# Optimization experiments

Measured on AMD Instinct MI355X. Metric: run time of the kernel, lower is better.

The kernel has to match this reference:

```python
import jax, jax.numpy as jnp
import numpy as np
from jax import lax

DIM = 192
HEADS = 8
B, H, W = 8, 128, 128


def dwconv3x3(x, w):
    # x: [B,C,H,W], w: [C,1,3,3] depthwise (groups=C)
    return lax.conv_general_dilated(
        x, w, window_strides=(1, 1), padding='SAME',
        feature_group_count=x.shape[1],
        dimension_numbers=('NCHW', 'OIHW', 'NCHW'))


def conv1x1(x, w, b=None):
    # w: [Cout, Cin]
    y = jnp.einsum('oc,bchw->bohw', w, x)
    if b is not None:
        y = y + b[None, :, None, None]
    return y


def setup_inputs() -> dict:
    key = jax.random.key(0)
    ks = jax.random.split(key, 9)
    s = 0.02
    return {
        'x': jax.random.normal(ks[0], (B, DIM, H, W), jnp.float32),
        'w_qkv': jax.random.normal(ks[1], (3 * DIM, DIM), jnp.float32) * s,
        'b_qkv': jnp.zeros((3 * DIM,), jnp.float32),
        'w_dw': jax.random.normal(ks[2], (3 * DIM, 1, 3, 3), jnp.float32) * s,
        'b_dw': jnp.zeros((3 * DIM,), jnp.float32),
        'w_proj': jax.random.normal(ks[3], (DIM, DIM), jnp.float32) * s,
        'b_proj': jnp.zeros((DIM,), jnp.float32),
        'w_pos1': jax.random.normal(ks[4], (DIM, 1, 3, 3), jnp.float32) * s,
        'w_pos2': jax.random.normal(ks[5], (DIM, 1, 3, 3), jnp.float32) * s,
        'temperature': jnp.ones((HEADS, 1, 1), jnp.float32),
    }


def reference(x, w_qkv, b_qkv, w_dw, b_dw, w_proj, b_proj, w_pos1, w_pos2, temperature):
    b, c, h, w = x.shape
    heads = HEADS
    ch = c // heads

    qkv = conv1x1(x, w_qkv, b_qkv)
    qkv = dwconv3x3(qkv, w_dw) + b_dw[None, :, None, None]
    q_inp, k_inp, v_inp = jnp.split(qkv, 3, axis=1)

    def to_heads(t):  # [B,C,H,W] -> [B,heads,ch,HW]
        return t.reshape(b, heads, ch, h * w)

    q = to_heads(q_inp)
    k = to_heads(k_inp)
    v = to_heads(v_inp)

    # L2 normalize over hw (torch F.normalize, eps=1e-12)
    q = q / jnp.maximum(jnp.linalg.norm(q, axis=-1, keepdims=True), 1e-12)
    k = k / jnp.maximum(jnp.linalg.norm(k, axis=-1, keepdims=True), 1e-12)

    attn = jnp.einsum('bhce,bhde->bhcd', q, k) * temperature  # [B,heads,ch,ch]
    attn = jax.nn.softmax(attn, axis=-1)
    out = jnp.einsum('bhcd,bhde->bhce', attn, v)  # [B,heads,ch,HW]
    out = out.reshape(b, c, h, w)

    out = conv1x1(out, w_proj, b_proj)

    pos = dwconv3x3(v_inp, w_pos1)
    pos = jax.nn.gelu(pos, approximate=False)
    pos = dwconv3x3(pos, w_pos2)

    return out + pos
```

## Files before the change

### kernel.cpp

```cpp
#include <hip/hip_runtime.h>
#include <stdint.h>
#include <stddef.h>

#define NB 8
#define CC 192
#define C3 576
#define HGT 128
#define WID 128
#define HW 16384
#define NH 8
#define QKROW 49152

typedef short bf16x8 __attribute__((ext_vector_type(8)));
typedef float f32x4 __attribute__((ext_vector_type(4)));

__device__ __forceinline__ unsigned short f2bf(float f) {
  unsigned int u = __float_as_uint(f);
  u += 0x7fffu + ((u >> 16) & 1u);
  return (unsigned short)(u >> 16);
}
__device__ __forceinline__ float bf2f(unsigned short h) {
  return __uint_as_float(((unsigned int)h) << 16);
}
__device__ __forceinline__ float bflo(unsigned int v) {
  return __uint_as_float(v << 16);
}
__device__ __forceinline__ float bfhi(unsigned int v) {
  return __uint_as_float(v & 0xffff0000u);
}
__device__ __forceinline__ unsigned int pk2(float a, float b) {
  return (unsigned int)f2bf(a) | ((unsigned int)f2bf(b) << 16);
}
__device__ __forceinline__ void gl_lds16(const void* g, void* l) {
  __builtin_amdgcn_global_load_lds(
      (const __attribute__((address_space(1))) unsigned int*)(uintptr_t)g,
      (__attribute__((address_space(3))) unsigned int*)(uint32_t)(uintptr_t)l,
      16, 0, 0);
}
__device__ __forceinline__ int xcd_swz(int g, int n) {
  return (g & 7) * (n >> 3) + (g >> 3);
}

__global__ void kwprep(const float* __restrict__ wq, unsigned char* __restrict__ wb) {
  int f = blockIdx.x * 256 + threadIdx.x;
  if (f >= C3 * 24) return;
  int oc = f / 24, s = f % 24;
  unsigned int wv[4];
#pragma unroll
  for (int j = 0; j < 4; ++j)
    wv[j] = pk2(wq[oc * 192 + s * 8 + 2 * j], wq[oc * 192 + s * 8 + 2 * j + 1]);
  uint4 st; st.x = wv[0]; st.y = wv[1]; st.z = wv[2]; st.w = wv[3];
  *(uint4*)(wb + (size_t)oc * 384 + ((s ^ (oc & 7)) * 16)) = st;
}

__global__ __launch_bounds__(256) void kqkv(const float* __restrict__ x,
                                            const unsigned char* __restrict__ wb,
                                            const float* __restrict__ bqkv,
                                            unsigned short* __restrict__ vout,
                                            unsigned char* __restrict__ qkout) {
  __shared__ __align__(16) unsigned char lds[81920];
  const int ABF = 49152;
  const int TRO = 73728;
  int wg = xcd_swz(blockIdx.x, gridDim.x);
  int t = wg & 255, b = wg >> 8;
  int p0 = t * 64;
  int tid = threadIdx.x;

  const unsigned char* gx = (const unsigned char*)(x + (size_t)b * CC * HW + p0);
#pragma unroll
  for (int i = 0; i < 12; ++i) {
    int f = i * 256 + tid;
    int ch = f >> 4, seg = f & 15;
    gl_lds16(gx + ((size_t)ch * HW + seg * 4) * 4, lds + f * 16);
  }
  asm volatile("s_waitcnt vmcnt(0)" ::: "memory");
  __syncthreads();
  {
    const float* lx = (const float*)lds;
    int p = tid & 63, sg = tid >> 6;
#pragma unroll
    for (int s6 = 0; s6 < 6; ++s6) {
      int s = sg * 6 + s6;
      unsigned int wv[4];
#pragma unroll
      for (int j = 0; j < 4; ++j)
        wv[j] = pk2(lx[(s * 8 + 2 * j) * 64 + p], lx[(s * 8 + 2 * j + 1) * 64 + p]);
      uint4 st; st.x = wv[0]; st.y = wv[1]; st.z = wv[2]; st.w = wv[3];
      *(uint4*)(lds + ABF + (s * 64 + p) * 16) = st;
    }
  }
  __syncthreads();

#pragma unroll
  for (int i = 0; i < 6; ++i)
    gl_lds16(wb + i * 4096 + tid * 16, lds + i * 4096 + tid * 16);

  int lane = tid & 63, w = tid >> 6;
  int l15 = lane & 15, gq = lane >> 4;
  int pw = w * 16;
  int y = t >> 1, xh = (t & 1) * 8;
  int unitw = w * 2 + (gq >> 1);
  int sub8 = (gq & 1) * 8;
  int s4 = w * 4 + gq;
  int ru = tid >> 5, rc0 = tid & 31;
  int vc = tid >> 2, vxq = tid & 3;

  for (int ot = 0; ot < 9; ++ot) {
    if (ot == 0) { asm volatile("s_waitcnt vmcnt(0)" ::: "memory"); }
    else         { asm volatile("s_waitcnt vmcnt(2)" ::: "memory"); }
    __builtin_amdgcn_s_barrier();
    __builtin_amdgcn_sched_barrier(0);
    int nb = ot & 1;
    float bias[4];
#pragma unroll
    for (int nf = 0; nf < 4; ++nf) bias[nf] = bqkv[ot * 64 + nf * 16 + l15];
    if (ot < 8) {
      const unsigned char* gB = wb + (size_t)(ot + 1) * 24576;
#pragma unroll
      for (int i = 0; i < 6; ++i)
        gl_lds16(gB + i * 4096 + tid * 16, lds + (nb ^ 1) * 24576 + i * 4096 + tid * 16);
    }
    f32x4 acc[4];
#pragma unroll
    for (int nf = 0; nf < 4; ++nf) acc[nf] = (f32x4){0.f, 0.f, 0.f, 0.f};
#pragma unroll
    for (int kk = 0; kk < 6; ++kk) {
      bf16x8 a = *(const bf16x8*)(lds + ABF + (((kk * 4 + gq) * 64) + pw + l15) * 16);
      int cb = kk * 64 + gq * 16;
#pragma unroll
      for (int nf = 0; nf < 4; ++nf) {
        int r = nf * 16 + l15;
        bf16x8 bfr = *(const bf16x8*)(lds + nb * 24576 + r * 384 + (cb ^ ((r & 7) << 4)));
        acc[nf] = __builtin_amdgcn_mfma_f32_16x16x32_bf16(a, bfr, acc[nf], 0, 0, 0);
      }
    }
    bool isq = (ot < 6);
    if (isq) {
#pragma unroll
      for (int nf = 0; nf < 4; ++nf) {
        int c = nf * 16 + l15;
        uint2 st;
        st.x = pk2(acc[nf][0] + bias[nf], acc[nf][1] + bias[nf]);
        st.y = pk2(acc[nf][2] + bias[nf], acc[nf][3] + bias[nf]);
        *(uint2*)(lds + TRO + c * 128 + ((unitw ^ (c & 7)) * 16) + sub8) = st;
      }
    } else {
#pragma unroll
      for (int nf = 0; nf < 4; ++nf) {
        int c = nf * 16 + l15;
        uint2 st;
        st.x = pk2(acc[nf][0] + bias[nf], acc[nf][1] + bias[nf]);
        st.y = pk2(acc[nf][2] + bias[nf], acc[nf][3] + bias[nf]);
        *(uint2*)(lds + TRO + c * 128 + ((s4 ^ (c & 15)) * 8)) = st;
      }
    }
    asm volatile("s_waitcnt lgkmcnt(0)" ::: "memory");
    __builtin_amdgcn_s_barrier();
    __builtin_amdgcn_sched_barrier(0);
    if (isq) {
      int part = ot / 3, cm0 = (ot % 3) * 64;
      int c1 = rc0 + 32;
      uint4 v0 = *(const uint4*)(lds + TRO + rc0 * 128 + ((ru ^ (rc0 & 7)) * 16));
      uint4 v1 = *(const uint4*)(lds + TRO + c1 * 128 + ((ru ^ (c1 & 7)) * 16));
      unsigned char* grow = qkout + ((size_t)((part * 8 + b) * 128 + y)) * QKROW +
                            (xh + ru) * 3072 + cm0 * 16;
      *(uint4*)(grow + rc0 * 16) = v0;
      *(uint4*)(grow + c1 * 16) = v1;
    } else {
      uint2 q0 = *(const uint2*)(lds + TRO + vc * 128 + (((4 * vxq + 0) ^ (vc & 15)) * 8));
      uint2 q1 = *(const uint2*)(lds + TRO + vc * 128 + (((4 * vxq + 1) ^ (vc & 15)) * 8));
      uint2 q2 = *(const uint2*)(lds + TRO + vc * 128 + (((4 * vxq + 2) ^ (vc & 15)) * 8));
      uint2 q3 = *(const uint2*)(lds + TRO + vc * 128 + (((4 * vxq + 3) ^ (vc & 15)) * 8));
      unsigned short* vp = vout + ((size_t)(b * CC + (ot - 6) * 64 + vc)) * HW + p0 + vxq * 16;
      uint4 s0; s0.x = q0.x; s0.y = q0.y; s0.z = q1.x; s0.w = q1.y;
      uint4 s1; s1.x = q2.x; s1.y = q2.y; s1.z = q3.x; s1.w = q3.y;
      *(uint4*)vp = s0;
      *(uint4*)(vp + 8) = s1;
    }
  }
}

__global__ __launch_bounds__(256) void kqk(const unsigned char* __restrict__ qk,
                                           const float* __restrict__ wdw,
                                           const float* __restrict__ bdw,
                                           float* __restrict__ G,
                                           float* __restrict__ nq,
                                           float* __restrict__ nk) {
  __shared__ __align__(16) unsigned char lds[49168];
  const int FB = 0;
  const int ZP = 24576;
  const int STG = 24592;
  int wg = xcd_swz(blockIdx.x, gridDim.x);
  int band = wg & 63, h = (wg >> 6) & 7, b = wg >> 9;
  int y0 = band * 2;
  int tid = threadIdx.x;
  if (tid == 0) *(uint4*)(lds + ZP) = (uint4){0, 0, 0, 0};

  int lane = tid & 63, w = tid >> 6;
  int ch = tid >> 3, row = (tid >> 2) & 1, qt = tid & 3;
  int u0 = qt * 4;

#pragma unroll
  for (int p = 0; p < 2; ++p) {
#pragma unroll
    for (int i = 0; i < 6; ++i) {
      int f = i * 256 + tid;
      int r = f / 384, unit = f % 384;
      int uc = unit / 24, cs = unit % 24;
      int yy = y0 - 1 + r;
      if (yy >= 0 && yy < HGT)
        gl_lds16(qk + ((size_t)((p * 8 + b) * 128 + yy)) * QKROW + uc * 3072 + (h * 24 + cs) * 16,
                 lds + STG + f * 16);
      else
        *(uint4*)(lds + STG + f * 16) = (uint4){0, 0, 0, 0};
    }
    asm volatile("s_waitcnt vmcnt(0)" ::: "memory");
    __syncthreads();
    if (tid < 192) {
      int gc = p * 192 + h * 24 + ch;
      float wv[9];
#pragma unroll
      for (int j = 0; j < 9; ++j) wv[j] = wdw[gc * 9 + j];
      float bias = bdw[gc];
      const unsigned char* sbase = lds + STG + ch * 16;
      unsigned char* fb = lds + FB + p * 12288 + (row * 4 + qt) * 1536 + ch * 16;
      unsigned int W[3][16];
#define LOADU3(dy_, m_, u_) { \
    uint4 tt = ((u_) >= 0 && (u_) < 16) \
        ? *(const uint4*)(sbase + (row + (dy_)) * 6144 + (u_) * 384) \
        : (uint4){0, 0, 0, 0}; \
    W[dy_][(m_) * 4 + 0] = tt.x; W[dy_][(m_) * 4 + 1] = tt.y; \
    W[dy_][(m_) * 4 + 2] = tt.z; W[dy_][(m_) * 4 + 3] = tt.w; }
#pragma unroll
      for (int dy = 0; dy < 3; ++dy) {
#pragma unroll
        for (int m = 0; m < 4; ++m) { LOADU3(dy, m, u0 - 1 + m); }
      }
      float nsum = 0.f;
#pragma unroll
      for (int c4 = 0; c4 < 2; ++c4) {
        if (c4 > 0) {
#pragma unroll
          for (int dy = 0; dy < 3; ++dy) {
#pragma unroll
            for (int e = 0; e < 8; ++e) W[dy][e] = W[dy][8 + e];
            LOADU3(dy, 2, u0 + 3);
            LOADU3(dy, 3, u0 + 4);
          }
        }
        float acc[16];
#pragma unroll
        for (int j = 0; j < 16; ++j) acc[j] = bias;
#pragma unroll
        for (int dy = 0; dy < 3; ++dy) {
          float f[18];
#pragma unroll
          for (int t2 = 0; t2 < 18; ++t2) {
            int rel = 7 + t2;
            unsigned int v = W[dy][rel >> 1];
            f[t2] = (rel & 1) ? bfhi(v) : bflo(v);
          }
#pragma unroll
          for (int j = 0; j < 16; ++j)
            acc[j] += f[j] * wv[dy * 3] + f[j + 1] * wv[dy * 3 + 1] + f[j + 2] * wv[dy * 3 + 2];
        }
#pragma unroll
        for (int j = 0; j < 16; ++j) nsum += acc[j] * acc[j];
        unsigned int pk[8];
#pragma unroll
        for (int e = 0; e < 8; ++e) pk[e] = pk2(acc[2 * e], acc[2 * e + 1]);
        uint4 s0; s0.x = pk[0]; s0.y = pk[1]; s0.z = pk[2]; s0.w = pk[3];
        uint4 s1; s1.x = pk[4]; s1.y = pk[5]; s1.z = pk[6]; s1.w = pk[7];
        *(uint4*)(fb + (c4 * 2) * 384) = s0;
        *(uint4*)(fb + (c4 * 2 + 1) * 384) = s1;
      }
#undef LOADU3
      nsum += __shfl_xor(nsum, 1);
      nsum += __shfl_xor(nsum, 2);
      nsum += __shfl_xor(nsum, 4);
      if ((tid & 7) == 0) {
        float* dst = (p == 0) ? nq : nk;
        atomicAdd(dst + (b * NH + h) * 24 + ch, nsum);
      }
    }
    __syncthreads();
  }

  int l15 = lane & 15, gq = lane >> 4;
  f32x4 acc2[2][2];
#pragma unroll
  for (int ct = 0; ct < 2; ++ct)
#pragma unroll
    for (int dt = 0; dt < 2; ++dt) acc2[ct][dt] = (f32x4){0.f, 0.f, 0.f, 0.f};
#pragma unroll
  for (int t2 = 0; t2 < 2; ++t2) {
    int kt = w * 2 + t2;
    bf16x8 aq[2], bk[2];
#pragma unroll
    for (int ct = 0; ct < 2; ++ct) {
      int c = ct * 16 + l15;
      const unsigned char* qa =
          (c < 24) ? (lds + FB + kt * 1536 + gq * 384 + c * 16) : (lds + ZP);
      const unsigned char* ka =
          (c < 24) ? (lds + FB + 12288 + kt * 1536 + gq * 384 + c * 16) : (lds + ZP);
      aq[ct] = *(const bf16x8*)qa;
      bk[ct] = *(const bf16x8*)ka;
    }
#pragma unroll
    for (int ct = 0; ct < 2; ++ct)
#pragma unroll
      for (int dt = 0; dt < 2; ++dt)
        acc2[ct][dt] = __builtin_amdgcn_mfma_f32_16x16x32_bf16(aq[ct], bk[dt], acc2[ct][dt], 0, 0, 0);
  }
  float* gp = (float*)(lds + STG);
#pragma unroll
  for (int ct = 0; ct < 2; ++ct)
#pragma unroll
    for (int dt = 0; dt < 2; ++dt)
      *(f32x4*)(gp + (((w * 4 + ct * 2 + dt) * 64) + lane) * 4) = acc2[ct][dt];
  __syncthreads();
  float* Gb = G + (size_t)(b * NH + h) * 576;
#pragma unroll
  for (int ii = 0; ii < 3; ++ii) {
    int f = ii * 256 + tid;
    if (f < 576) {
      int c = f / 24, d = f % 24;
      int t4 = ((c >> 4) << 1) + (d >> 4);
      int lane16 = (d & 15) + (((c & 15) >> 2) << 4);
      int reg = c & 3;
      float s = 0.f;
#pragma unroll
      for (int w4 = 0; w4 < 4; ++w4)
        s += gp[((w4 * 4 + t4) * 64 + lane16) * 4 + reg];
      atomicAdd(Gb + f, s);
    }
  }
}

__global__ __launch_bounds__(256) void kdwv(const unsigned short* __restrict__ src,
                                            const float* __restrict__ wdw,
                                            const float* __restrict__ bdw,
                                            unsigned char* __restrict__ vT) {
  __shared__ __align__(16) unsigned int smem[8 * 721];
  int wg = xcd_swz(blockIdx.x, gridDim.x);
  int cg = wg % 24, rt = (wg / 24) & 15, b = wg / 384;
  int y0 = rt * 8, chg0 = cg * 8;
  int tid = threadIdx.x;
  for (int i = tid; i < 5768; i += 256) smem[i] = 0;
  __syncthreads();
#pragma unroll
  for (int i = 0; i < 5; ++i) {
    int f = i * 256 + tid;
    int ch = f / 160, rem = f % 160;
    int r = rem >> 4, seg = rem & 15;
    int y = y0 - 1 + r;
    if (y >= 0 && y < HGT) {
      uint4 v = *(const uint4*)(src + ((size_t)(b * CC + chg0 + ch)) * HW + y * WID + seg * 8);
      unsigned int* dp = smem + ch * 721 + r * 72 + 4 + seg * 4;
      dp[0] = v.x; dp[1] = v.y; dp[2] = v.z; dp[3] = v.w;
    }
  }
  __syncthreads();
  int ch = tid >> 5, u = tid & 31;
  int row = u >> 2, xs = (u & 3) * 32;
  int gch = 384 + chg0 + ch;
  float wv[9];
#pragma unroll
  for (int j = 0; j < 9; ++j) wv[j] = wdw[gch * 9 + j];
  float bias = bdw[gch];
  float outv[32];
  const unsigned int* tb = smem + ch * 721;
#pragma unroll
  for (int g = 0; g < 4; ++g) {
    int x0 = xs + g * 8;
    float v[3][12];
#pragma unroll
    for (int dy = 0; dy < 3; ++dy) {
      const unsigned int* rp = tb + (row + dy) * 72 + ((x0 + 6) >> 1);
#pragma unroll
      for (int m = 0; m < 6; ++m) {
        unsigned int w2 = rp[m];
        v[dy][2 * m] = bf2f((unsigned short)(w2 & 0xffff));
        v[dy][2 * m + 1] = bf2f((unsigned short)(w2 >> 16));
      }
    }
#pragma unroll
    for (int j = 0; j < 8; ++j) {
      float a = bias;
#pragma unroll
      for (int dy = 0; dy < 3; ++dy)
#pragma unroll
        for (int dx = 0; dx < 3; ++dx)
          a += v[dy][j + dx + 1] * wv[dy * 3 + dx];
      outv[g * 8 + j] = a;
    }
  }
  __syncthreads();
  unsigned short* vt = (unsigned short*)smem;
#pragma unroll
  for (int g = 0; g < 4; ++g)
#pragma unroll
    for (int j = 0; j < 8; j += 2) {
      int x = xs + g * 8 + j;
      ((unsigned int*)smem)[ch * 512 + row * 64 + (x >> 1)] =
          pk2(outv[g * 8 + j], outv[g * 8 + j + 1]);
    }
  __syncthreads();
#pragma unroll
  for (int i = 0; i < 4; ++i) {
    int f = i * 256 + tid;
    int r = f >> 7, col = f & 127;
    unsigned int wvp[4];
#pragma unroll
    for (int e = 0; e < 4; ++e) {
      unsigned short a = vt[(2 * e) * 1024 + r * 128 + col];
      unsigned short bb = vt[(2 * e + 1) * 1024 + r * 128 + col];
      wvp[e] = (unsigned int)a | ((unsigned int)bb << 16);
    }
    uint4 st; st.x = wvp[0]; st.y = wvp[1]; st.z = wvp[2]; st.w = wvp[3];
    *(uint4*)(vT + (((size_t)(b * 24 + cg)) * HW + (size_t)(y0 + r) * WID + col) * 16) = st;
  }
}

__global__ __launch_bounds__(256) void kattn(const float* __restrict__ G,
                                             const float* __restrict__ nq,
                                             const float* __restrict__ nk,
                                             const float* __restrict__ temp,
                                             const float* __restrict__ wproj,
                                             unsigned char* __restrict__ W2) {
  __shared__ float attn[24][24];
  __shared__ float iq[24], ik[24];
  int bh = blockIdx.x;
  int h = bh & 7, b = bh >> 3;
  int tid = threadIdx.x;
  const float* Gb = G + (size_t)bh * 576;
  if (tid < 24) { float n = sqrtf(nq[bh * 24 + tid]); iq[tid] = 1.f / fmaxf(n, 1e-12f); }
  else if (tid < 48) { float n = sqrtf(nk[bh * 24 + tid - 24]); ik[tid - 24] = 1.f / fmaxf(n, 1e-12f); }
  __syncthreads();
  if (tid < 24) {
    float tmp = temp[h];
    float row[24];
    float mx = -1e30f;
#pragma unroll
    for (int d = 0; d < 24; ++d) {
      row[d] = Gb[tid * 24 + d] * iq[tid] * ik[d] * tmp;
      mx = fmaxf(mx, row[d]);
    }
    float sum = 0.f;
#pragma unroll
    for (int d = 0; d < 24; ++d) { float e = expf(row[d] - mx); row[d] = e; sum += e; }
    float inv = 1.f / sum;
#pragma unroll
    for (int d = 0; d < 24; ++d) attn[tid][d] = row[d] * inv;
  }
  __syncthreads();
  for (int i = 0; i < 18; ++i) {
    int f = tid + i * 256;
    if (f >= 4608) break;
    int oc = f / 24, d = f % 24;
    float s = 0.f;
#pragma unroll
    for (int c = 0; c < 24; ++c) s += wproj[oc * 192 + h * 24 + c] * attn[c][d];
    int gg = h * 24 + d;
    *(unsigned short*)(W2 + ((size_t)b * CC + oc) * 384 + ((gg * 2) ^ ((oc & 7) << 4))) = f2bf(s);
  }
}

__global__ __launch_bounds__(256) void kpos(const unsigned char* __restrict__ vT,
                                            const float* __restrict__ w1,
                                            const float* __restrict__ w2,
                                            unsigned short* __restrict__ pos) {
  __shared__ unsigned int vbuf[8 * 865];
  __shared__ unsigned int d1[8 * 721];
  int wg = xcd_swz(blockIdx.x, gridDim.x);
  int cg = wg % 24, rt = (wg / 24) & 15, b = wg / 384;
  int y0 = rt * 8, g0 = cg * 8;
  int tid = threadIdx.x;
  for (int i = tid; i < 6920; i += 256) vbuf[i] = 0;
  __syncthreads();
#pragma unroll
  for (int i = 0; i < 3; ++i) {
    int f = i * 256 + tid;
    int r = f >> 6, colp = f & 63;
    int y = y0 - 2 + r;
    if (y >= 0 && y < HGT) {
      const unsigned char* base = vT + (((size_t)(b * 24 + cg)) * HW + (size_t)y * WID + colp * 2) * 16;
      uint4 va = *(const uint4*)(base);
      uint4 vb2 = *(const uint4*)(base + 16);
      unsigned int la[4] = {va.x, va.y, va.z, va.w};
      unsigned int lb[4] = {vb2.x, vb2.y, vb2.z, vb2.w};
#pragma unroll
      for (int e = 0; e < 8; ++e) {
        unsigned int a16 = (la[e >> 1] >> ((e & 1) * 16)) & 0xffff;
        unsigned int b16 = (lb[e >> 1] >> ((e & 1) * 16)) & 0xffff;
        vbuf[e * 865 + r * 72 + colp + 4] = a16 | (b16 << 16);
      }
    }
  }
  __syncthreads();
  int ch = tid >> 5, u = tid & 31;
  {
    const float* wp = w1 + (g0 + ch) * 9;
    float wl[9];
#pragma unroll
    for (int j = 0; j < 9; ++j) wl[j] = wp[j];
    int x0 = u * 4;
    for (int rr = 0; rr < 10; ++rr) {
      int y = y0 - 1 + rr;
      unsigned int o0 = 0, o1 = 0;
      if (y >= 0 && y < HGT) {
        float v[3][8];
#pragma unroll
        for (int dy = 0; dy < 3; ++dy) {
          const unsigned int* rp = vbuf + ch * 865 + (rr + dy) * 72 + ((x0 + 6) >> 1);
#pragma unroll
          for (int m = 0; m < 4; ++m) {
            unsigned int w2r = rp[m];
            v[dy][2 * m] = bf2f((unsigned short)(w2r & 0xffff));
            v[dy][2 * m + 1] = bf2f((unsigned short)(w2r >> 16));
          }
        }
        float g4[4];
#pragma unroll
        for (int j = 0; j < 4; ++j) {
          float a = 0.f;
#pragma unroll
          for (int dy = 0; dy < 3; ++dy)
#pragma unroll
            for (int dx = 0; dx < 3; ++dx)
              a += v[dy][j + dx + 1] * wl[dy * 3 + dx];
          g4[j] = 0.5f * a * (1.f + erff(a * 0.70710678118f));
        }
        o0 = pk2(g4[0], g4[1]);
        o1 = pk2(g4[2], g4[3]);
      }
      unsigned int* dp = d1 + ch * 721 + rr * 72 + ((x0 + 8) >> 1);
      dp[0] = o0; dp[1] = o1;
    }
  }
  if (tid < 160) {
    int ech = tid / 20, rem = tid % 20;
    int rr = rem >> 1, side = rem & 1;
    int x = side ? 128 : -1;
    int y = y0 - 1 + rr;
    unsigned short val = 0;
    if (y >= 0 && y < HGT) {
      const float* wp = w1 + (g0 + ech) * 9;
      float a = 0.f;
      const unsigned short* vb16 = (const unsigned short*)(vbuf + ech * 865);
#pragma unroll
      for (int dy = 0; dy < 3; ++dy)
#pragma unroll
        for (int dx = 0; dx < 3; ++dx)
          a += bf2f(vb16[(rr + dy) * 144 + (x + dx + 7)]) * wp[dy * 3 + dx];
      val = f2bf(0.5f * a * (1.f + erff(a * 0.70710678118f)));
    }
    ((unsigned short*)(d1 + ech * 721))[rr * 144 + (x + 8)] = val;
  }
  __syncthreads();
  {
    const float* wp = w2 + (g0 + ch) * 9;
    float wl[9];
#pragma unroll
    for (int j = 0; j < 9; ++j) wl[j] = wp[j];
    int row = u >> 2, xs = (u & 3) * 32;
    size_t rb = ((size_t)(b * CC + g0 + ch)) * HW + (size_t)(y0 + row) * WID;
#pragma unroll
    for (int g = 0; g < 4; ++g) {
      int x0 = xs + g * 8;
      float v[3][12];
#pragma unroll
      for (int dy = 0; dy < 3; ++dy) {
        const unsigned int* rp = d1 + ch * 721 + (row + dy) * 72 + ((x0 + 6) >> 1);
#pragma unroll
        for (int m = 0; m < 6; ++m) {
          unsigned int w2r = rp[m];
          v[dy][2 * m] = bf2f((unsigned short)(w2r & 0xffff));
          v[dy][2 * m + 1] = bf2f((unsigned short)(w2r >> 16));
        }
      }
      uint4 st;
      float o[8];
#pragma unroll
      for (int j = 0; j < 8; ++j) {
        float a = 0.f;
#pragma unroll
        for (int dy = 0; dy < 3; ++dy)
#pragma unroll
          for (int dx = 0; dx < 3; ++dx)
            a += v[dy][j + dx + 1] * wl[dy * 3 + dx];
        o[j] = a;
      }
      st.x = pk2(o[0], o[1]); st.y = pk2(o[2], o[3]);
      st.z = pk2(o[4], o[5]); st.w = pk2(o[6], o[7]);
      *(uint4*)(pos + rb + x0) = st;
    }
  }
}

__global__ __launch_bounds__(256) void kproj(const unsigned char* __restrict__ vT,
                                             const unsigned char* __restrict__ W2,
                                             const float* __restrict__ bproj,
                                             const unsigned short* __restrict__ pos,
                                             float* __restrict__ out) {
  __shared__ __align__(16) unsigned char lds[73728];
  int wg = xcd_swz(blockIdx.x, gridDim.x);
  int ot = wg % 3; int rest = wg / 3; int grp = rest & 63; int b = rest >> 6;
  int tid = threadIdx.x;
  const unsigned char* gB = W2 + ((size_t)(b * 192 + ot * 64)) * 384;
#pragma unroll
  for (int i = 0; i < 6; ++i)
    gl_lds16(gB + i * 4096 + tid * 16, lds + 49152 + i * 4096 + tid * 16);
  const unsigned char* gA = vT + (size_t)b * 24 * HW * 16;
  int t0 = grp * 4;
  {
    int p0 = t0 * 64;
#pragma unroll
    for (int i = 0; i < 6; ++i) {
      int f = i * 256 + tid;
      gl_lds16(gA + (((size_t)(f >> 6)) * HW + p0 + (f & 63)) * 16, lds + f * 16);
    }
  }
  int lane = tid & 63, w = tid >> 6;
  int l15 = lane & 15, gq = lane >> 4;
  int pw = w * 16;
  float bias[4];
  size_t obase[4];
#pragma unroll
  for (int nf = 0; nf < 4; ++nf) {
    int oc = ot * 64 + nf * 16 + l15;
    bias[nf] = bproj[oc];
    obase[nf] = ((size_t)(b * 192 + oc)) * HW;
  }
  for (int it = 0; it < 4; ++it) {
    int tile = t0 + it;
    asm volatile("s_waitcnt vmcnt(0)" ::: "memory");
    __syncthreads();
    int nb = it & 1;
    if (it < 3) {
      int p1 = (tile + 1) * 64;
#pragma unroll
      for (int i = 0; i < 6; ++i) {
        int f = i * 256 + tid;
        gl_lds16(gA + (((size_t)(f >> 6)) * HW + p1 + (f & 63)) * 16,
                 lds + ((nb ^ 1) * 24576) + f * 16);
      }
    }
    f32x4 acc[4];
#pragma unroll
    for (int nf = 0; nf < 4; ++nf) acc[nf] = (f32x4){0.f, 0.f, 0.f, 0.f};
#pragma unroll
    for (int kk = 0; kk < 6; ++kk) {
      bf16x8 a = *(const bf16x8*)(lds + nb * 24576 + ((((kk * 4 + gq) << 6) + pw + l15) * 16));
      int cb = kk * 64 + gq * 16;
#pragma unroll
      for (int nf = 0; nf < 4; ++nf) {
        int r = nf * 16 + l15;
        bf16x8 bfr = *(const bf16x8*)(lds + 49152 + r * 384 + (cb ^ ((r & 7) << 4)));
        acc[nf] = __builtin_amdgcn_mfma_f32_16x16x32_bf16(a, bfr, acc[nf], 0, 0, 0);
      }
    }
    int p = tile * 64 + pw + gq * 4;
#pragma unroll
    for (int nf = 0; nf < 4; ++nf) {
      uint2 pv = *(const uint2*)(pos + obase[nf] + p);
      float4 o;
      o.x = acc[nf][0] + bias[nf] + bf2f((unsigned short)(pv.x & 0xffff));
      o.y = acc[nf][1] + bias[nf] + bf2f((unsigned short)(pv.x >> 16));
      o.z = acc[nf][2] + bias[nf] + bf2f((unsigned short)(pv.y & 0xffff));
      o.w = acc[nf][3] + bias[nf] + bf2f((unsigned short)(pv.y >> 16));
      *(float4*)(out + obase[nf] + p) = o;
    }
  }
}

#define OFF_W   ((size_t)0)
#define OFF_G   ((size_t)221184)
#define OFF_NQ  ((size_t)368640)
#define OFF_NK  ((size_t)374784)
#define OFF_W2  ((size_t)380928)
#define OFF_QK  ((size_t)970752)
#define OFF_V   ((size_t)101634048)
#define OFF_XT  ((size_t)151965696)

extern "C" void kernel_launch(void* const* d_in, const int* in_sizes, int n_in,
                              void* d_out, int out_size, void* d_ws, size_t ws_size,
                              hipStream_t stream) {
  const float* x     = (const float*)d_in[0];
  const float* wqkv  = (const float*)d_in[1];
  const float* bqkv  = (const float*)d_in[2];
  const float* wdw   = (const float*)d_in[3];
  const float* bdw   = (const float*)d_in[4];
  const float* wproj = (const float*)d_in[5];
  const float* bproj = (const float*)d_in[6];
  const float* wpos1 = (const float*)d_in[7];
  const float* wpos2 = (const float*)d_in[8];
  const float* temp  = (const float*)d_in[9];
  unsigned char* ws = (unsigned char*)d_ws;

  hipMemsetAsync(ws + OFF_G, 0, 147456 + 6144 + 6144, stream);
  kwprep<<<54, 256, 0, stream>>>(wqkv, ws + OFF_W);
  kqkv<<<2048, 256, 0, stream>>>(x, ws + OFF_W, bqkv,
                                 (unsigned short*)(ws + OFF_V), ws + OFF_QK);
  kqk<<<4096, 256, 0, stream>>>(ws + OFF_QK, wdw, bdw, (float*)(ws + OFF_G),
                                (float*)(ws + OFF_NQ), (float*)(ws + OFF_NK));
  kdwv<<<3072, 256, 0, stream>>>((const unsigned short*)(ws + OFF_V), wdw, bdw,
                                 ws + OFF_XT);
  kattn<<<64, 256, 0, stream>>>((const float*)(ws + OFF_G), (const float*)(ws + OFF_NQ),
                                (const float*)(ws + OFF_NK), temp, wproj, ws + OFF_W2);
  kpos<<<3072, 256, 0, stream>>>(ws + OFF_XT, wpos1, wpos2,
                                 (unsigned short*)(ws + OFF_QK));
  kproj<<<1536, 256, 0, stream>>>(ws + OFF_XT, ws + OFF_W2, bproj,
                                  (const unsigned short*)(ws + OFF_QK), (float*)d_out);
}
```

Baseline: 287.8 us.

## Shrink kqkv LDS footprint, prefetch pos early in kproj, fold memset into kwprep

kqkv now stages the input in two 96-channel chunks and splits each weight tile into half-tiles of 32 output channels with 3 loads each. This cuts shared memory from 80KB to 52KB so more workgroups fit per CU, at the price of twice as many loop iterations and barriers. kproj now issues the pos loads before the MFMA loop and uses a partial vmcnt wait, hiding global latency. The hipMemsetAsync is replaced by zero stores inside kwprep, removing one launch.

```diff
diff --git a/kernel.cpp b/kernel.cpp
--- a/kernel.cpp
+++ b/kernel.cpp
@@ -41,8 +41,10 @@
   return (g & 7) * (n >> 3) + (g >> 3);
 }
 
-__global__ void kwprep(const float* __restrict__ wq, unsigned char* __restrict__ wb) {
+__global__ void kwprep(const float* __restrict__ wq, unsigned char* __restrict__ wb,
+                       unsigned char* __restrict__ zero_region) {
   int f = blockIdx.x * 256 + threadIdx.x;
+  if (f < 9984) *(uint4*)(zero_region + (size_t)f * 16) = (uint4){0, 0, 0, 0};
   if (f >= C3 * 24) return;
   int oc = f / 24, s = f % 24;
   unsigned int wv[4];
@@ -58,42 +60,43 @@
                                             const float* __restrict__ bqkv,
                                             unsigned short* __restrict__ vout,
                                             unsigned char* __restrict__ qkout) {
-  __shared__ __align__(16) unsigned char lds[81920];
-  const int ABF = 49152;
-  const int TRO = 73728;
+  __shared__ __align__(16) unsigned char lds[53248];
+  const int ABF = 0;
+  const int BB  = 24576;
+  const int TR  = 49152;
   int wg = xcd_swz(blockIdx.x, gridDim.x);
   int t = wg & 255, b = wg >> 8;
   int p0 = t * 64;
   int tid = threadIdx.x;
-
   const unsigned char* gx = (const unsigned char*)(x + (size_t)b * CC * HW + p0);
-#pragma unroll
-  for (int i = 0; i < 12; ++i) {
-    int f = i * 256 + tid;
-    int ch = f >> 4, seg = f & 15;
-    gl_lds16(gx + ((size_t)ch * HW + seg * 4) * 4, lds + f * 16);
-  }
-  asm volatile("s_waitcnt vmcnt(0)" ::: "memory");
-  __syncthreads();
-  {
-    const float* lx = (const float*)lds;
-    int p = tid & 63, sg = tid >> 6;
-#pragma unroll
-    for (int s6 = 0; s6 < 6; ++s6) {
-      int s = sg * 6 + s6;
+
+  int p = tid & 63, sg = tid >> 6;
+#pragma unroll
+  for (int ck = 0; ck < 2; ++ck) {
+#pragma unroll
+    for (int i = 0; i < 6; ++i) {
+      int f = i * 256 + tid;
+      int ch = ck * 96 + (f >> 4), seg = f & 15;
+      gl_lds16(gx + ((size_t)ch * HW + seg * 4) * 4, lds + BB + f * 16);
+    }
+    asm volatile("s_waitcnt vmcnt(0)" ::: "memory");
+    __syncthreads();
+    const float* lx = (const float*)(lds + BB);
+#pragma unroll
+    for (int s3 = 0; s3 < 3; ++s3) {
+      int s = sg * 3 + s3;
       unsigned int wv[4];
 #pragma unroll
       for (int j = 0; j < 4; ++j)
         wv[j] = pk2(lx[(s * 8 + 2 * j) * 64 + p], lx[(s * 8 + 2 * j + 1) * 64 + p]);
       uint4 st; st.x = wv[0]; st.y = wv[1]; st.z = wv[2]; st.w = wv[3];
-      *(uint4*)(lds + ABF + (s * 64 + p) * 16) = st;
-    }
-  }
-  __syncthreads();
-
-#pragma unroll
-  for (int i = 0; i < 6; ++i)
-    gl_lds16(wb + i * 4096 + tid * 16, lds + i * 4096 + tid * 16);
+      *(uint4*)(lds + ABF + ((ck * 12 + s) * 64 + p) * 16) = st;
+    }
+    __syncthreads();
+  }
+#pragma unroll
+  for (int i = 0; i < 3; ++i)
+    gl_lds16(wb + i * 4096 + tid * 16, lds + BB + i * 4096 + tid * 16);
 
   int lane = tid & 63, w = tid >> 6;
   int l15 = lane & 15, gq = lane >> 4;
@@ -102,80 +105,74 @@
   int unitw = w * 2 + (gq >> 1);
   int sub8 = (gq & 1) * 8;
   int s4 = w * 4 + gq;
-  int ru = tid >> 5, rc0 = tid & 31;
-  int vc = tid >> 2, vxq = tid & 3;
-
-  for (int ot = 0; ot < 9; ++ot) {
-    if (ot == 0) { asm volatile("s_waitcnt vmcnt(0)" ::: "memory"); }
-    else         { asm volatile("s_waitcnt vmcnt(2)" ::: "memory"); }
+  int tc = tid & 31, tu = tid >> 5;
+  int vcv = tid >> 3, vx = tid & 7;
+
+  for (int j = 0; j < 18; ++j) {
+    int ot = j >> 1, hh = j & 1, cur = j & 1;
+    if (j == 0) { asm volatile("s_waitcnt vmcnt(0)" ::: "memory"); }
+    else        { asm volatile("s_waitcnt vmcnt(1)" ::: "memory"); }
     __builtin_amdgcn_s_barrier();
     __builtin_amdgcn_sched_barrier(0);
-    int nb = ot & 1;
-    float bias[4];
-#pragma unroll
-    for (int nf = 0; nf < 4; ++nf) bias[nf] = bqkv[ot * 64 + nf * 16 + l15];
-    if (ot < 8) {
-      const unsigned char* gB = wb + (size_t)(ot + 1) * 24576;
-#pragma unroll
-      for (int i = 0; i < 6; ++i)
-        gl_lds16(gB + i * 4096 + tid * 16, lds + (nb ^ 1) * 24576 + i * 4096 + tid * 16);
-    }
-    f32x4 acc[4];
-#pragma unroll
-    for (int nf = 0; nf < 4; ++nf) acc[nf] = (f32x4){0.f, 0.f, 0.f, 0.f};
+    float bias0 = bqkv[ot * 64 + hh * 32 + l15];
+    float bias1 = bqkv[ot * 64 + hh * 32 + 16 + l15];
+    if (j < 17) {
+      int jn = j + 1;
+      const unsigned char* gB = wb + (size_t)(jn >> 1) * 24576 + (jn & 1) * 12288;
+#pragma unroll
+      for (int i = 0; i < 3; ++i)
+        gl_lds16(gB + i * 4096 + tid * 16, lds + BB + (cur ^ 1) * 12288 + i * 4096 + tid * 16);
+    }
+    f32x4 acc[2];
+    acc[0] = (f32x4){0.f, 0.f, 0.f, 0.f};
+    acc[1] = (f32x4){0.f, 0.f, 0.f, 0.f};
 #pragma unroll
     for (int kk = 0; kk < 6; ++kk) {
       bf16x8 a = *(const bf16x8*)(lds + ABF + (((kk * 4 + gq) * 64) + pw + l15) * 16);
       int cb = kk * 64 + gq * 16;
 #pragma unroll
-      for (int nf = 0; nf < 4; ++nf) {
-        int r = nf * 16 + l15;
-        bf16x8 bfr = *(const bf16x8*)(lds + nb * 24576 + r * 384 + (cb ^ ((r & 7) << 4)));
-        acc[nf] = __builtin_amdgcn_mfma_f32_16x16x32_bf16(a, bfr, acc[nf], 0, 0, 0);
+      for (int nf2 = 0; nf2 < 2; ++nf2) {
+        int r2 = nf2 * 16 + l15;
+        bf16x8 bfr = *(const bf16x8*)(lds + BB + cur * 12288 + r2 * 384 + (cb ^ ((r2 & 7) << 4)));
+        acc[nf2] = __builtin_amdgcn_mfma_f32_16x16x32_bf16(a, bfr, acc[nf2], 0, 0, 0);
       }
     }
     bool isq = (ot < 6);
     if (isq) {
 #pragma unroll
-      for (int nf = 0; nf < 4; ++nf) {
-        int c = nf * 16 + l15;
+      for (int nf2 = 0; nf2 < 2; ++nf2) {
+        int c = nf2 * 16 + l15;
+        float bs = nf2 ? bias1 : bias0;
         uint2 st;
-        st.x = pk2(acc[nf][0] + bias[nf], acc[nf][1] + bias[nf]);
-        st.y = pk2(acc[nf][2] + bias[nf], acc[nf][3] + bias[nf]);
-        *(uint2*)(lds + TRO + c * 128 + ((unitw ^ (c & 7)) * 16) + sub8) = st;
+        st.x = pk2(acc[nf2][0] + bs, acc[nf2][1] + bs);
+        st.y = pk2(acc[nf2][2] + bs, acc[nf2][3] + bs);
+        *(uint2*)(lds + TR + c * 128 + ((unitw ^ (c & 7)) * 16) + sub8) = st;
       }
     } else {
 #pragma unroll
-      for (int nf = 0; nf < 4; ++nf) {
-        int c = nf * 16 + l15;
+      for (int nf2 = 0; nf2 < 2; ++nf2) {
+        int c = nf2 * 16 + l15;
+        float bs = nf2 ? bias1 : bias0;
         uint2 st;
-        st.x = pk2(acc[nf][0] + bias[nf], acc[nf][1] + bias[nf]);
-        st.y = pk2(acc[nf][2] + bias[nf], acc[nf][3] + bias[nf]);
-        *(uint2*)(lds + TRO + c * 128 + ((s4 ^ (c & 15)) * 8)) = st;
+        st.x = pk2(acc[nf2][0] + bs, acc[nf2][1] + bs);
+        st.y = pk2(acc[nf2][2] + bs, acc[nf2][3] + bs);
+        *(uint2*)(lds + TR + c * 128 + ((s4 ^ (c & 15)) * 8)) = st;
       }
     }
     asm volatile("s_waitcnt lgkmcnt(0)" ::: "memory");
     __builtin_amdgcn_s_barrier();
     __builtin_amdgcn_sched_barrier(0);
     if (isq) {
-      int part = ot / 3, cm0 = (ot % 3) * 64;
-      int c1 = rc0 + 32;
-      uint4 v0 = *(const uint4*)(lds + TRO + rc0 * 128 + ((ru ^ (rc0 & 7)) * 16));
-      uint4 v1 = *(const uint4*)(lds + TRO + c1 * 128 + ((ru ^ (c1 & 7)) * 16));
-      unsigned char* grow = qkout + ((size_t)((part * 8 + b) * 128 + y)) * QKROW +
-                            (xh + ru) * 3072 + cm0 * 16;
-      *(uint4*)(grow + rc0 * 16) = v0;
-      *(uint4*)(grow + c1 * 16) = v1;
+      int part = ot / 3, cm = (ot % 3) * 64 + hh * 32 + tc;
+      uint4 v0 = *(const uint4*)(lds + TR + tc * 128 + ((tu ^ (tc & 7)) * 16));
+      *(uint4*)(qkout + ((size_t)((part * 8 + b) * 128 + y)) * QKROW +
+                (xh + tu) * 3072 + cm * 16) = v0;
     } else {
-      uint2 q0 = *(const uint2*)(lds + TRO + vc * 128 + (((4 * vxq + 0) ^ (vc & 15)) * 8));
-      uint2 q1 = *(const uint2*)(lds + TRO + vc * 128 + (((4 * vxq + 1) ^ (vc & 15)) * 8));
-      uint2 q2 = *(const uint2*)(lds + TRO + vc * 128 + (((4 * vxq + 2) ^ (vc & 15)) * 8));
-      uint2 q3 = *(const uint2*)(lds + TRO + vc * 128 + (((4 * vxq + 3) ^ (vc & 15)) * 8));
-      unsigned short* vp = vout + ((size_t)(b * CC + (ot - 6) * 64 + vc)) * HW + p0 + vxq * 16;
+      uint2 q0 = *(const uint2*)(lds + TR + vcv * 128 + (((2 * vx) ^ (vcv & 15)) * 8));
+      uint2 q1 = *(const uint2*)(lds + TR + vcv * 128 + (((2 * vx + 1) ^ (vcv & 15)) * 8));
       uint4 s0; s0.x = q0.x; s0.y = q0.y; s0.z = q1.x; s0.w = q1.y;
-      uint4 s1; s1.x = q2.x; s1.y = q2.y; s1.z = q3.x; s1.w = q3.y;
-      *(uint4*)vp = s0;
-      *(uint4*)(vp + 8) = s1;
+      *(uint4*)(vout + ((size_t)(b * CC + (ot - 6) * 64 + hh * 32 + vcv)) * HW +
+                p0 + vx * 8) = s0;
     }
   }
 }
@@ -634,9 +631,16 @@
   }
   for (int it = 0; it < 4; ++it) {
     int tile = t0 + it;
-    asm volatile("s_waitcnt vmcnt(0)" ::: "memory");
-    __syncthreads();
+    if (it == 0) { asm volatile("s_waitcnt vmcnt(0)" ::: "memory"); }
+    else         { asm volatile("s_waitcnt vmcnt(4)" ::: "memory"); }
+    __builtin_amdgcn_s_barrier();
+    __builtin_amdgcn_sched_barrier(0);
     int nb = it & 1;
+    int p = tile * 64 + pw + gq * 4;
+    uint2 pv[4];
+#pragma unroll
+    for (int nf = 0; nf < 4; ++nf)
+      pv[nf] = *(const uint2*)(pos + obase[nf] + p);
     if (it < 3) {
       int p1 = (tile + 1) * 64;
 #pragma unroll
@@ -646,6 +650,7 @@
                  lds + ((nb ^ 1) * 24576) + f * 16);
       }
     }
+    __builtin_amdgcn_sched_barrier(0);
     f32x4 acc[4];
 #pragma unroll
     for (int nf = 0; nf < 4; ++nf) acc[nf] = (f32x4){0.f, 0.f, 0.f, 0.f};
@@ -660,15 +665,13 @@
         acc[nf] = __builtin_amdgcn_mfma_f32_16x16x32_bf16(a, bfr, acc[nf], 0, 0, 0);
       }
     }
-    int p = tile * 64 + pw + gq * 4;
 #pragma unroll
     for (int nf = 0; nf < 4; ++nf) {
-      uint2 pv = *(const uint2*)(pos + obase[nf] + p);
       float4 o;
-      o.x = acc[nf][0] + bias[nf] + bf2f((unsigned short)(pv.x & 0xffff));
-      o.y = acc[nf][1] + bias[nf] + bf2f((unsigned short)(pv.x >> 16));
-      o.z = acc[nf][2] + bias[nf] + bf2f((unsigned short)(pv.y & 0xffff));
-      o.w = acc[nf][3] + bias[nf] + bf2f((unsigned short)(pv.y >> 16));
+      o.x = acc[nf][0] + bias[nf] + bf2f((unsigned short)(pv[nf].x & 0xffff));
+      o.y = acc[nf][1] + bias[nf] + bf2f((unsigned short)(pv[nf].x >> 16));
+      o.z = acc[nf][2] + bias[nf] + bf2f((unsigned short)(pv[nf].y & 0xffff));
+      o.w = acc[nf][3] + bias[nf] + bf2f((unsigned short)(pv[nf].y >> 16));
       *(float4*)(out + obase[nf] + p) = o;
     }
   }
@@ -698,8 +701,7 @@
   const float* temp  = (const float*)d_in[9];
   unsigned char* ws = (unsigned char*)d_ws;
 
-  hipMemsetAsync(ws + OFF_G, 0, 147456 + 6144 + 6144, stream);
-  kwprep<<<54, 256, 0, stream>>>(wqkv, ws + OFF_W);
+  kwprep<<<54, 256, 0, stream>>>(wqkv, ws + OFF_W, ws + OFF_G);
   kqkv<<<2048, 256, 0, stream>>>(x, ws + OFF_W, bqkv,
                                  (unsigned short*)(ws + OFF_V), ws + OFF_QK);
   kqk<<<4096, 256, 0, stream>>>(ws + OFF_QK, wdw, bdw, (float*)(ws + OFF_G),
```

Result: no change. 285.6 us (median of 2 runs) (-0.8%).
